# Kernel optimization log

Hardware: AMD Instinct MI355X
Metric: run time of the kernel (lower is better)

## Reference

```python
import jax, jax.numpy as jnp
import numpy as np

ALPHA = 0.1
DEPTH = 10
N_NODES = 100000
N_EDGES = 1600000
FEATS = 512
HIDDEN = 64
CLASSES = 64


def setup_inputs() -> dict:
    key = jax.random.key(0)
    k1, k2, k3, k4 = jax.random.split(key, 4)
    x = jax.random.normal(k1, (N_NODES, FEATS), dtype=jnp.float32)
    edges = jax.random.randint(k2, (2, N_EDGES), 0, N_NODES, dtype=jnp.int64)
    W1 = jax.random.normal(k3, (FEATS, HIDDEN), dtype=jnp.float32) * (1.0 / np.sqrt(FEATS))
    b1 = jnp.zeros((HIDDEN,), dtype=jnp.float32)
    W2 = jax.random.normal(k4, (HIDDEN, CLASSES), dtype=jnp.float32) * (1.0 / np.sqrt(HIDDEN))
    b2 = jnp.zeros((CLASSES,), dtype=jnp.float32)
    return {"x": x, "edges": edges, "W1": W1, "b1": b1, "W2": W2, "b2": b2}


def reference(x, edges, W1, b1, W2, b2):
    src, dst = edges[0], edges[1]
    # symmetric GCN normalization from edge list (in-degree over dst)
    deg = jax.ops.segment_sum(jnp.ones((N_EDGES,), jnp.float32), dst,
                              num_segments=N_NODES)
    deg = jnp.maximum(deg, 1.0)
    inv_sqrt_deg = jax.lax.rsqrt(deg)
    norm = inv_sqrt_deg[src] * inv_sqrt_deg[dst]  # [E]

    # MLP: feats -> hidden -> classes (dropout = identity in eval mode)
    h = jax.nn.relu(x @ W1 + b1)
    h = h @ W2 + b2
    h0 = h

    for _ in range(DEPTH):
        msgs = h[src] * norm[:, None]                     # [E, C] gather
        agg = jax.ops.segment_sum(msgs, dst, num_segments=N_NODES)  # scatter-add
        h = agg * (1.0 - ALPHA) + ALPHA * h0
    return h
```

## Files before the change

kernel.cpp:

```cpp
#include <hip/hip_runtime.h>
#include <hip/hip_fp16.h>

#define FEATS 512
#define HIDDEN 64
#define CLASSES 64
#define DEPTH 10
#define ALPHA 0.1f

#define BUCKET_BITS 8
#define BUCKET 256
#define NB_C 391
#define K3_CHUNK 8192
#define K3_THREADS 512

typedef __attribute__((ext_vector_type(8))) short short8;
typedef __attribute__((ext_vector_type(4))) float f32x4;

__device__ __forceinline__ unsigned short bf16_hi(float f) {
    unsigned u = __float_as_uint(f);
    unsigned r = u + 0x7FFF + ((u >> 16) & 1);
    return (unsigned short)(r >> 16);
}
__device__ __forceinline__ float bf16_tof(unsigned short h) {
    return __uint_as_float(((unsigned)h) << 16);
}

__global__ __launch_bounds__(256) void bucket_hist_kernel(const int* __restrict__ dst,
                                                          int* __restrict__ bcnt,
                                                          int NB, int E) {
    __shared__ int h[NB_C];
    for (int j = threadIdx.x; j < NB; j += 256) h[j] = 0;
    __syncthreads();
    int i = blockIdx.x * 256 + threadIdx.x;
    int stride = gridDim.x * 256;
    for (; i < E; i += stride) atomicAdd(&h[dst[i] >> BUCKET_BITS], 1);
    __syncthreads();
    for (int j = threadIdx.x; j < NB; j += 256) {
        int v = h[j];
        if (v) atomicAdd(&bcnt[j], v);
    }
}

__global__ __launch_bounds__(1024) void bucket_scan_kernel(const int* __restrict__ bcnt,
                                                           int* __restrict__ bptr,
                                                           int* __restrict__ gcur,
                                                           int* __restrict__ rowptr,
                                                           int NB, int N, int E) {
    __shared__ int sd[1024];
    int t = threadIdx.x;
    int i0 = 2 * t, i1 = 2 * t + 1;
    int a = (i0 < NB) ? bcnt[i0] : 0;
    int b = (i1 < NB) ? bcnt[i1] : 0;
    int s = a + b;
    sd[t] = s;
    __syncthreads();
    for (int off = 1; off < 1024; off <<= 1) {
        int v = (t >= off) ? sd[t - off] : 0;
        __syncthreads();
        sd[t] += v;
        __syncthreads();
    }
    int excl = sd[t] - s;
    if (i0 < NB) { bptr[i0] = excl;     gcur[i0] = excl; }
    if (i1 < NB) { bptr[i1] = excl + a; gcur[i1] = excl + a; }
    if (t == 0) { bptr[NB] = E; rowptr[N] = E; }
}

__global__ __launch_bounds__(K3_THREADS) void bucket_scatter_kernel(const int* __restrict__ src,
                                                                    const int* __restrict__ dst,
                                                                    int* __restrict__ gcur,
                                                                    int* __restrict__ part,
                                                                    int NB, int E) {
    __shared__ int hist[NB_C];
    __shared__ int base[NB_C];
    int cbase = blockIdx.x * K3_CHUNK;
    for (int j = threadIdx.x; j < NB; j += K3_THREADS) hist[j] = 0;
    __syncthreads();
    for (int k = 0; k < K3_CHUNK; k += K3_THREADS) {
        int i = cbase + k + threadIdx.x;
        if (i < E) atomicAdd(&hist[dst[i] >> BUCKET_BITS], 1);
    }
    __syncthreads();
    for (int j = threadIdx.x; j < NB; j += K3_THREADS) {
        int h = hist[j];
        base[j] = (h > 0) ? atomicAdd(&gcur[j], h) : 0;
        hist[j] = 0;
    }
    __syncthreads();
    for (int k = 0; k < K3_CHUNK; k += K3_THREADS) {
        int i = cbase + k + threadIdx.x;
        if (i < E) {
            int d = dst[i];
            int j = d >> BUCKET_BITS;
            int off = atomicAdd(&hist[j], 1);
            part[(size_t)(base[j] + off)] = (src[i] << BUCKET_BITS) | (d & (BUCKET - 1));
        }
    }
}

__global__ __launch_bounds__(256) void part_to_csr_kernel(const int* __restrict__ bptr,
                                                          const int* __restrict__ part,
                                                          int* __restrict__ rowptr,
                                                          float* __restrict__ inv_sqrt,
                                                          int* __restrict__ csr_src,
                                                          int N) {
    __shared__ int cnt[BUCKET];
    __shared__ int cur[BUCKET];
    __shared__ int wsum[4];
    int b = blockIdx.x;
    int lo = b << BUCKET_BITS;
    int tid = threadIdx.x;
    int p0 = bptr[b], p1 = bptr[b + 1];
    cnt[tid] = 0;
    __syncthreads();
    for (int i = p0 + tid; i < p1; i += 256) {
        atomicAdd(&cnt[part[i] & (BUCKET - 1)], 1);
    }
    __syncthreads();
    {
        int wv = tid >> 6, ln = tid & 63;
        int v = cnt[tid];
        int incl = v;
#pragma unroll
        for (int off = 1; off < 64; off <<= 1) {
            int t = __shfl_up(incl, off);
            if (ln >= off) incl += t;
        }
        if (ln == 63) wsum[wv] = incl;
        __syncthreads();
        int woff = 0;
#pragma unroll
        for (int w = 0; w < 4; ++w)
            if (w < wv) woff += wsum[w];
        int excl = woff + incl - v;
        if (lo + tid < N) {
            rowptr[lo + tid] = p0 + excl;
            inv_sqrt[lo + tid] = rsqrtf((float)(v < 1 ? 1 : v));
        }
        cur[tid] = excl;
    }
    __syncthreads();
    for (int i = p0 + tid; i < p1; i += 256) {
        int pe = part[i];
        int off = atomicAdd(&cur[pe & (BUCKET - 1)], 1);
        csr_src[p0 + off] = ((unsigned)pe) >> BUCKET_BITS;
    }
}

__global__ __launch_bounds__(256) void pack_w_kernel(const float* __restrict__ W1,
                                                     const float* __restrict__ W2,
                                                     unsigned short* __restrict__ w1h,
                                                     unsigned short* __restrict__ w1l,
                                                     unsigned short* __restrict__ w2h,
                                                     unsigned short* __restrict__ w2l) {
    int id = blockIdx.x * blockDim.x + threadIdx.x;
    if (id < 4096) {
        int lane = id & 63, f = (id >> 6) & 3, ks = id >> 8;
        int col = f * 16 + (lane & 15);
        int k0 = ks * 32 + (lane >> 4) * 8;
#pragma unroll
        for (int i = 0; i < 8; ++i) {
            float v = W1[(k0 + i) * HIDDEN + col];
            unsigned short h = bf16_hi(v);
            w1h[id * 8 + i] = h;
            w1l[id * 8 + i] = bf16_hi(v - bf16_tof(h));
        }
    } else if (id < 4096 + 512) {
        int p = id - 4096;
        int lane = p & 63, f = (p >> 6) & 3, ks = p >> 8;
        int col = f * 16 + (lane & 15);
        int k0 = ks * 32 + (lane >> 4) * 8;
#pragma unroll
        for (int i = 0; i < 8; ++i) {
            float v = W2[(k0 + i) * CLASSES + col];
            unsigned short h = bf16_hi(v);
            w2h[p * 8 + i] = h;
            w2l[p * 8 + i] = bf16_hi(v - bf16_tof(h));
        }
    }
}

__global__ __launch_bounds__(256) void mlp_mfma_kernel(const float* __restrict__ x,
                                                       const unsigned short* __restrict__ w1h,
                                                       const unsigned short* __restrict__ w1l,
                                                       const float* __restrict__ b1,
                                                       const unsigned short* __restrict__ w2h,
                                                       const unsigned short* __restrict__ w2l,
                                                       const float* __restrict__ b2,
                                                       const float* __restrict__ is,
                                                       __half* __restrict__ h0h,
                                                       __half* __restrict__ u0,
                                                       int N) {
    __shared__ float hs[4][16][68];
    int wave = threadIdx.x >> 6;
    int lane = threadIdx.x & 63;
    int tile = blockIdx.x * 4 + wave;
    if (tile * 16 >= N) return;

    int row = lane & 15;
    int koff = (lane >> 4) * 8;
    const short8* w1hv = (const short8*)w1h;
    const short8* w1lv = (const short8*)w1l;
    const short8* w2hv = (const short8*)w2h;
    const short8* w2lv = (const short8*)w2l;

    f32x4 c[4] = {};
    const float* xrow = x + (size_t)(tile * 16 + row) * FEATS + koff;
#pragma unroll 4
    for (int ks = 0; ks < 16; ++ks) {
        float4 a0 = *(const float4*)(xrow + ks * 32);
        float4 a1 = *(const float4*)(xrow + ks * 32 + 4);
        float av[8] = {a0.x, a0.y, a0.z, a0.w, a1.x, a1.y, a1.z, a1.w};
        short8 ah, al;
#pragma unroll
        for (int j = 0; j < 8; ++j) {
            unsigned short h = bf16_hi(av[j]);
            ah[j] = (short)h;
            al[j] = (short)bf16_hi(av[j] - bf16_tof(h));
        }
#pragma unroll
        for (int f = 0; f < 4; ++f) {
            short8 bh = w1hv[(ks * 4 + f) * 64 + lane];
            short8 bl = w1lv[(ks * 4 + f) * 64 + lane];
            c[f] = __builtin_amdgcn_mfma_f32_16x16x32_bf16(ah, bh, c[f], 0, 0, 0);
            c[f] = __builtin_amdgcn_mfma_f32_16x16x32_bf16(ah, bl, c[f], 0, 0, 0);
            c[f] = __builtin_amdgcn_mfma_f32_16x16x32_bf16(al, bh, c[f], 0, 0, 0);
        }
    }
#pragma unroll
    for (int f = 0; f < 4; ++f) {
        float bias = b1[f * 16 + (lane & 15)];
#pragma unroll
        for (int r = 0; r < 4; ++r) {
            hs[wave][(lane >> 4) * 4 + r][f * 16 + (lane & 15)] = fmaxf(c[f][r] + bias, 0.0f);
        }
    }

    f32x4 c2[4] = {};
#pragma unroll
    for (int ks = 0; ks < 2; ++ks) {
        float4 a0 = *(const float4*)&hs[wave][row][ks * 32 + koff];
        float4 a1 = *(const float4*)&hs[wave][row][ks * 32 + koff + 4];
        float av[8] = {a0.x, a0.y, a0.z, a0.w, a1.x, a1.y, a1.z, a1.w};
        short8 ah, al;
#pragma unroll
        for (int j = 0; j < 8; ++j) {
            unsigned short h = bf16_hi(av[j]);
            ah[j] = (short)h;
            al[j] = (short)bf16_hi(av[j] - bf16_tof(h));
        }
#pragma unroll
        for (int f = 0; f < 4; ++f) {
            short8 bh = w2hv[(ks * 4 + f) * 64 + lane];
            short8 bl = w2lv[(ks * 4 + f) * 64 + lane];
            c2[f] = __builtin_amdgcn_mfma_f32_16x16x32_bf16(ah, bh, c2[f], 0, 0, 0);
            c2[f] = __builtin_amdgcn_mfma_f32_16x16x32_bf16(ah, bl, c2[f], 0, 0, 0);
            c2[f] = __builtin_amdgcn_mfma_f32_16x16x32_bf16(al, bh, c2[f], 0, 0, 0);
        }
    }
    float isv[4];
#pragma unroll
    for (int r = 0; r < 4; ++r) {
        int n = tile * 16 + (lane >> 4) * 4 + r;
        isv[r] = is[n];
    }
#pragma unroll
    for (int f = 0; f < 4; ++f) {
        float bias = b2[f * 16 + (lane & 15)];
#pragma unroll
        for (int r = 0; r < 4; ++r) {
            int n = tile * 16 + (lane >> 4) * 4 + r;
            float v = c2[f][r] + bias;
            h0h[(size_t)n * CLASSES + f * 16 + (lane & 15)] = __float2half(v);
            u0[(size_t)n * CLASSES + f * 16 + (lane & 15)] = __float2half(v * isv[r]);
        }
    }
}

__global__ __launch_bounds__(256) void prop_kernel(const int* __restrict__ rowptr,
                                                   const int* __restrict__ csr_src,
                                                   const float* __restrict__ is,
                                                   const __half* __restrict__ u_in,
                                                   const __half* __restrict__ h0h,
                                                   __half* __restrict__ u_out,
                                                   float* __restrict__ out_f32,
                                                   int N, int last) {
    int wid = (blockIdx.x * blockDim.x + threadIdx.x) >> 6;
    int lane = threadIdx.x & 63;
    if (wid >= N) return;
    int base = rowptr[wid];
    int end = rowptr[wid + 1];
    int grp = lane >> 3, sub = lane & 7;

    float isd = is[wid];
    size_t rowo = ((size_t)wid << 6) + (sub << 3);
    uint4 hq = make_uint4(0, 0, 0, 0);
    if (grp == 0) hq = *(const uint4*)(h0h + rowo);

    float acc[8] = {0.f, 0.f, 0.f, 0.f, 0.f, 0.f, 0.f, 0.f};
    for (int b = base; b < end; b += 16) {
        int e0 = b + grp;
        int e1 = e0 + 8;
        bool v0 = e0 < end;
        bool v1 = e1 < end;
        uint4 q0, q1;
        int s0, s1;
        if (v0) s0 = csr_src[e0];
        if (v1) s1 = csr_src[e1];
        if (v0) q0 = *(const uint4*)(u_in + ((size_t)s0 << 6) + (sub << 3));
        if (v1) q1 = *(const uint4*)(u_in + ((size_t)s1 << 6) + (sub << 3));
        if (v0) {
            const __half2* hp = (const __half2*)&q0;
#pragma unroll
            for (int k = 0; k < 4; ++k) {
                float2 f2 = __half22float2(hp[k]);
                acc[2 * k] += f2.x;
                acc[2 * k + 1] += f2.y;
            }
        }
        if (v1) {
            const __half2* hp = (const __half2*)&q1;
#pragma unroll
            for (int k = 0; k < 4; ++k) {
                float2 f2 = __half22float2(hp[k]);
                acc[2 * k] += f2.x;
                acc[2 * k + 1] += f2.y;
            }
        }
    }
#pragma unroll
    for (int j = 0; j < 8; ++j) {
        acc[j] += __shfl_xor(acc[j], 8);
        acc[j] += __shfl_xor(acc[j], 16);
        acc[j] += __shfl_xor(acc[j], 32);
    }
    if (grp == 0) {
        const __half2* hp = (const __half2*)&hq;
        float h[8];
#pragma unroll
        for (int k = 0; k < 4; ++k) {
            float2 f2 = __half22float2(hp[k]);
            h[2 * k] = f2.x;
            h[2 * k + 1] = f2.y;
        }
        if (last) {
            float r[8];
#pragma unroll
            for (int j = 0; j < 8; ++j) r[j] = (1.0f - ALPHA) * isd * acc[j] + ALPHA * h[j];
            *(float4*)(out_f32 + rowo) = make_float4(r[0], r[1], r[2], r[3]);
            *(float4*)(out_f32 + rowo + 4) = make_float4(r[4], r[5], r[6], r[7]);
        } else {
            __half2 w[4];
#pragma unroll
            for (int k = 0; k < 4; ++k) {
                float a = ((1.0f - ALPHA) * isd * acc[2 * k] + ALPHA * h[2 * k]) * isd;
                float b = ((1.0f - ALPHA) * isd * acc[2 * k + 1] + ALPHA * h[2 * k + 1]) * isd;
                w[k] = __floats2half2_rn(a, b);
            }
            *(uint4*)(u_out + rowo) = *(uint4*)w;
        }
    }
}

extern "C" void kernel_launch(void* const* d_in, const int* in_sizes, int n_in,
                              void* d_out, int out_size, void* d_ws, size_t ws_size,
                              hipStream_t stream) {
    const float* x = (const float*)d_in[0];
    const int* edges = (const int*)d_in[1];
    const float* W1 = (const float*)d_in[2];
    const float* b1 = (const float*)d_in[3];
    const float* W2 = (const float*)d_in[4];
    const float* b2 = (const float*)d_in[5];
    float* out = (float*)d_out;

    const int N = in_sizes[0] / FEATS;
    const int E = in_sizes[1] / 2;
    const int NB = (N + BUCKET - 1) >> BUCKET_BITS;
    const int* src = edges;
    const int* dst = edges + E;

    char* ws = (char*)d_ws;
    size_t off = 0;
    auto alloc = [&](size_t bytes) {
        char* p = ws + off;
        off = (off + bytes + 255) & ~(size_t)255;
        return p;
    };
    int* part = (int*)alloc((size_t)E * 4);
    int* csr_src = (int*)alloc((size_t)E * 4);
    int* bcnt = (int*)alloc((size_t)NB * 4);
    int* bptr = (int*)alloc((size_t)(NB + 1) * 4);
    int* gcur = (int*)alloc((size_t)NB * 4);
    int* rowptr = (int*)alloc((size_t)(N + 1) * 4);
    float* inv_sqrt = (float*)alloc((size_t)N * 4);
    __half* h0h = (__half*)alloc((size_t)N * CLASSES * 2);
    __half* uA = (__half*)alloc((size_t)N * CLASSES * 2);
    __half* uB = (__half*)alloc((size_t)N * CLASSES * 2);
    unsigned short* w1h = (unsigned short*)alloc(4096 * 8 * 2);
    unsigned short* w1l = (unsigned short*)alloc(4096 * 8 * 2);
    unsigned short* w2h = (unsigned short*)alloc(512 * 8 * 2);
    unsigned short* w2l = (unsigned short*)alloc(512 * 8 * 2);
    (void)ws_size;

    hipMemsetAsync(bcnt, 0, (size_t)NB * 4, stream);
    bucket_hist_kernel<<<128, 256, 0, stream>>>(dst, bcnt, NB, E);
    bucket_scan_kernel<<<1, 1024, 0, stream>>>(bcnt, bptr, gcur, rowptr, NB, N, E);
    int k3_blocks = (E + K3_CHUNK - 1) / K3_CHUNK;
    bucket_scatter_kernel<<<k3_blocks, K3_THREADS, 0, stream>>>(src, dst, gcur, part, NB, E);
    part_to_csr_kernel<<<NB, 256, 0, stream>>>(bptr, part, rowptr, inv_sqrt, csr_src, N);

    pack_w_kernel<<<18, 256, 0, stream>>>(W1, W2, w1h, w1l, w2h, w2l);
    int tiles = (N + 15) / 16;
    mlp_mfma_kernel<<<(tiles + 3) / 4, 256, 0, stream>>>(x, w1h, w1l, b1, w2h, w2l, b2,
                                                         inv_sqrt, h0h, uA, N);

    int blocks = (N * 64 + 255) / 256;
    for (int d = 0; d < DEPTH; ++d) {
        const __half* uin = (d & 1) ? uB : uA;
        __half* uout = (d & 1) ? uA : uB;
        int last = (d == DEPTH - 1);
        prop_kernel<<<blocks, 256, 0, stream>>>(rowptr, csr_src, inv_sqrt, uin, h0h,
                                                uout, out, N, last);
    }
}
```

Baseline: 549.6 us.

## Partition CSR edges into source-range quarters for gather locality

Builds the CSR with an extra partition on source-node range (4 quarters of 32768 nodes), so edges are grouped by src quarter first and then by dst bucket. Each prop kernel wave walks four per-quarter row segments in turn, which is meant to keep the gathered u_in rows for a phase inside a smaller working set that fits better in L2/MALL cache. In exchange it adds a separate norm kernel, four times as many bucket counters and part_to_csr blocks, and more loop overhead and short segments per node in prop.

Result: slower. 790.0 us (+43.7%).

```diff
diff --git a/kernel.cpp b/kernel.cpp
--- a/kernel.cpp
+++ b/kernel.cpp
@@ -10,6 +10,9 @@
 #define BUCKET_BITS 8
 #define BUCKET 256
 #define NB_C 391
+#define NQT 4
+#define QT_SHIFT 15
+#define NK_C (NQT * NB_C)
 #define K3_CHUNK 8192
 #define K3_THREADS 512
 
@@ -25,17 +28,21 @@
     return __uint_as_float(((unsigned)h) << 16);
 }
 
-__global__ __launch_bounds__(256) void bucket_hist_kernel(const int* __restrict__ dst,
+__global__ __launch_bounds__(256) void bucket_hist_kernel(const int* __restrict__ src,
+                                                          const int* __restrict__ dst,
                                                           int* __restrict__ bcnt,
-                                                          int NB, int E) {
-    __shared__ int h[NB_C];
-    for (int j = threadIdx.x; j < NB; j += 256) h[j] = 0;
+                                                          int NB, int NK, int E) {
+    __shared__ int h[NK_C];
+    for (int j = threadIdx.x; j < NK; j += 256) h[j] = 0;
     __syncthreads();
     int i = blockIdx.x * 256 + threadIdx.x;
     int stride = gridDim.x * 256;
-    for (; i < E; i += stride) atomicAdd(&h[dst[i] >> BUCKET_BITS], 1);
-    __syncthreads();
-    for (int j = threadIdx.x; j < NB; j += 256) {
+    for (; i < E; i += stride) {
+        int kq = (src[i] >> QT_SHIFT) * NB + (dst[i] >> BUCKET_BITS);
+        atomicAdd(&h[kq], 1);
+    }
+    __syncthreads();
+    for (int j = threadIdx.x; j < NK; j += 256) {
         int v = h[j];
         if (v) atomicAdd(&bcnt[j], v);
     }
@@ -44,13 +51,13 @@
 __global__ __launch_bounds__(1024) void bucket_scan_kernel(const int* __restrict__ bcnt,
                                                            int* __restrict__ bptr,
                                                            int* __restrict__ gcur,
-                                                           int* __restrict__ rowptr,
-                                                           int NB, int N, int E) {
+                                                           int* __restrict__ rowq,
+                                                           int NB, int NK, int N, int E) {
     __shared__ int sd[1024];
     int t = threadIdx.x;
     int i0 = 2 * t, i1 = 2 * t + 1;
-    int a = (i0 < NB) ? bcnt[i0] : 0;
-    int b = (i1 < NB) ? bcnt[i1] : 0;
+    int a = (i0 < NK) ? bcnt[i0] : 0;
+    int b = (i1 < NK) ? bcnt[i1] : 0;
     int s = a + b;
     sd[t] = s;
     __syncthreads();
@@ -61,27 +68,32 @@
         __syncthreads();
     }
     int excl = sd[t] - s;
-    if (i0 < NB) { bptr[i0] = excl;     gcur[i0] = excl; }
-    if (i1 < NB) { bptr[i1] = excl + a; gcur[i1] = excl + a; }
-    if (t == 0) { bptr[NB] = E; rowptr[N] = E; }
+    if (i0 < NK) { bptr[i0] = excl;     gcur[i0] = excl; }
+    if (i1 < NK) { bptr[i1] = excl + a; gcur[i1] = excl + a; }
+    if (t == 0) bptr[NK] = E;
+    __syncthreads();
+    if (t < NQT) rowq[t * (N + 1) + N] = bptr[(t + 1) * NB];
 }
 
 __global__ __launch_bounds__(K3_THREADS) void bucket_scatter_kernel(const int* __restrict__ src,
                                                                     const int* __restrict__ dst,
                                                                     int* __restrict__ gcur,
                                                                     int* __restrict__ part,
-                                                                    int NB, int E) {
-    __shared__ int hist[NB_C];
-    __shared__ int base[NB_C];
+                                                                    int NB, int NK, int E) {
+    __shared__ int hist[NK_C];
+    __shared__ int base[NK_C];
     int cbase = blockIdx.x * K3_CHUNK;
-    for (int j = threadIdx.x; j < NB; j += K3_THREADS) hist[j] = 0;
+    for (int j = threadIdx.x; j < NK; j += K3_THREADS) hist[j] = 0;
     __syncthreads();
     for (int k = 0; k < K3_CHUNK; k += K3_THREADS) {
         int i = cbase + k + threadIdx.x;
-        if (i < E) atomicAdd(&hist[dst[i] >> BUCKET_BITS], 1);
-    }
-    __syncthreads();
-    for (int j = threadIdx.x; j < NB; j += K3_THREADS) {
+        if (i < E) {
+            int kq = (src[i] >> QT_SHIFT) * NB + (dst[i] >> BUCKET_BITS);
+            atomicAdd(&hist[kq], 1);
+        }
+    }
+    __syncthreads();
+    for (int j = threadIdx.x; j < NK; j += K3_THREADS) {
         int h = hist[j];
         base[j] = (h > 0) ? atomicAdd(&gcur[j], h) : 0;
         hist[j] = 0;
@@ -90,27 +102,28 @@
     for (int k = 0; k < K3_CHUNK; k += K3_THREADS) {
         int i = cbase + k + threadIdx.x;
         if (i < E) {
-            int d = dst[i];
-            int j = d >> BUCKET_BITS;
-            int off = atomicAdd(&hist[j], 1);
-            part[(size_t)(base[j] + off)] = (src[i] << BUCKET_BITS) | (d & (BUCKET - 1));
+            int sv = src[i], d = dst[i];
+            int kq = (sv >> QT_SHIFT) * NB + (d >> BUCKET_BITS);
+            int off = atomicAdd(&hist[kq], 1);
+            part[(size_t)(base[kq] + off)] = (sv << BUCKET_BITS) | (d & (BUCKET - 1));
         }
     }
 }
 
 __global__ __launch_bounds__(256) void part_to_csr_kernel(const int* __restrict__ bptr,
                                                           const int* __restrict__ part,
-                                                          int* __restrict__ rowptr,
-                                                          float* __restrict__ inv_sqrt,
+                                                          int* __restrict__ rowq,
                                                           int* __restrict__ csr_src,
-                                                          int N) {
+                                                          int NB, int N) {
     __shared__ int cnt[BUCKET];
     __shared__ int cur[BUCKET];
     __shared__ int wsum[4];
-    int b = blockIdx.x;
-    int lo = b << BUCKET_BITS;
+    int kb = blockIdx.x;
+    int qt = kb / NB;
+    int bb = kb - qt * NB;
+    int lo = bb << BUCKET_BITS;
     int tid = threadIdx.x;
-    int p0 = bptr[b], p1 = bptr[b + 1];
+    int p0 = bptr[kb], p1 = bptr[kb + 1];
     cnt[tid] = 0;
     __syncthreads();
     for (int i = p0 + tid; i < p1; i += 256) {
@@ -133,10 +146,7 @@
         for (int w = 0; w < 4; ++w)
             if (w < wv) woff += wsum[w];
         int excl = woff + incl - v;
-        if (lo + tid < N) {
-            rowptr[lo + tid] = p0 + excl;
-            inv_sqrt[lo + tid] = rsqrtf((float)(v < 1 ? 1 : v));
-        }
+        if (lo + tid < N) rowq[qt * (N + 1) + lo + tid] = p0 + excl;
         cur[tid] = excl;
     }
     __syncthreads();
@@ -145,6 +155,18 @@
         int off = atomicAdd(&cur[pe & (BUCKET - 1)], 1);
         csr_src[p0 + off] = ((unsigned)pe) >> BUCKET_BITS;
     }
+}
+
+__global__ __launch_bounds__(256) void norm_kernel(const int* __restrict__ rowq,
+                                                   float* __restrict__ inv_sqrt, int N) {
+    int i = blockIdx.x * 256 + threadIdx.x;
+    if (i >= N) return;
+    int deg = 0;
+#pragma unroll
+    for (int q = 0; q < NQT; ++q) {
+        deg += rowq[q * (N + 1) + i + 1] - rowq[q * (N + 1) + i];
+    }
+    inv_sqrt[i] = rsqrtf((float)(deg < 1 ? 1 : deg));
 }
 
 __global__ __launch_bounds__(256) void pack_w_kernel(const float* __restrict__ W1,
@@ -277,7 +299,7 @@
     }
 }
 
-__global__ __launch_bounds__(256) void prop_kernel(const int* __restrict__ rowptr,
+__global__ __launch_bounds__(256) void prop_kernel(const int* __restrict__ rowq,
                                                    const int* __restrict__ csr_src,
                                                    const float* __restrict__ is,
                                                    const __half* __restrict__ u_in,
@@ -288,8 +310,6 @@
     int wid = (blockIdx.x * blockDim.x + threadIdx.x) >> 6;
     int lane = threadIdx.x & 63;
     if (wid >= N) return;
-    int base = rowptr[wid];
-    int end = rowptr[wid + 1];
     int grp = lane >> 3, sub = lane & 7;
 
     float isd = is[wid];
@@ -298,33 +318,37 @@
     if (grp == 0) hq = *(const uint4*)(h0h + rowo);
 
     float acc[8] = {0.f, 0.f, 0.f, 0.f, 0.f, 0.f, 0.f, 0.f};
-    for (int b = base; b < end; b += 16) {
-        int e0 = b + grp;
-        int e1 = e0 + 8;
-        bool v0 = e0 < end;
-        bool v1 = e1 < end;
-        uint4 q0, q1;
-        int s0, s1;
-        if (v0) s0 = csr_src[e0];
-        if (v1) s1 = csr_src[e1];
-        if (v0) q0 = *(const uint4*)(u_in + ((size_t)s0 << 6) + (sub << 3));
-        if (v1) q1 = *(const uint4*)(u_in + ((size_t)s1 << 6) + (sub << 3));
-        if (v0) {
-            const __half2* hp = (const __half2*)&q0;
-#pragma unroll
-            for (int k = 0; k < 4; ++k) {
-                float2 f2 = __half22float2(hp[k]);
-                acc[2 * k] += f2.x;
-                acc[2 * k + 1] += f2.y;
+    for (int qt = 0; qt < NQT; ++qt) {
+        int base = rowq[qt * (N + 1) + wid];
+        int end = rowq[qt * (N + 1) + wid + 1];
+        for (int b = base; b < end; b += 16) {
+            int e0 = b + grp;
+            int e1 = e0 + 8;
+            bool v0 = e0 < end;
+            bool v1 = e1 < end;
+            uint4 q0, q1;
+            int s0, s1;
+            if (v0) s0 = csr_src[e0];
+            if (v1) s1 = csr_src[e1];
+            if (v0) q0 = *(const uint4*)(u_in + ((size_t)s0 << 6) + (sub << 3));
+            if (v1) q1 = *(const uint4*)(u_in + ((size_t)s1 << 6) + (sub << 3));
+            if (v0) {
+                const __half2* hp = (const __half2*)&q0;
+#pragma unroll
+                for (int k = 0; k < 4; ++k) {
+                    float2 f2 = __half22float2(hp[k]);
+                    acc[2 * k] += f2.x;
+                    acc[2 * k + 1] += f2.y;
+                }
             }
-        }
-        if (v1) {
-            const __half2* hp = (const __half2*)&q1;
-#pragma unroll
-            for (int k = 0; k < 4; ++k) {
-                float2 f2 = __half22float2(hp[k]);
-                acc[2 * k] += f2.x;
-                acc[2 * k + 1] += f2.y;
+            if (v1) {
+                const __half2* hp = (const __half2*)&q1;
+#pragma unroll
+                for (int k = 0; k < 4; ++k) {
+                    float2 f2 = __half22float2(hp[k]);
+                    acc[2 * k] += f2.x;
+                    acc[2 * k + 1] += f2.y;
+                }
             }
         }
     }
@@ -376,6 +400,7 @@
     const int N = in_sizes[0] / FEATS;
     const int E = in_sizes[1] / 2;
     const int NB = (N + BUCKET - 1) >> BUCKET_BITS;
+    const int NK = NQT * NB;
     const int* src = edges;
     const int* dst = edges + E;
 
@@ -388,10 +413,10 @@
     };
     int* part = (int*)alloc((size_t)E * 4);
     int* csr_src = (int*)alloc((size_t)E * 4);
-    int* bcnt = (int*)alloc((size_t)NB * 4);
-    int* bptr = (int*)alloc((size_t)(NB + 1) * 4);
-    int* gcur = (int*)alloc((size_t)NB * 4);
-    int* rowptr = (int*)alloc((size_t)(N + 1) * 4);
+    int* bcnt = (int*)alloc((size_t)NK * 4);
+    int* bptr = (int*)alloc((size_t)(NK + 1) * 4);
+    int* gcur = (int*)alloc((size_t)NK * 4);
+    int* rowq = (int*)alloc((size_t)NQT * (N + 1) * 4);
     float* inv_sqrt = (float*)alloc((size_t)N * 4);
     __half* h0h = (__half*)alloc((size_t)N * CLASSES * 2);
     __half* uA = (__half*)alloc((size_t)N * CLASSES * 2);
@@ -402,12 +427,13 @@
     unsigned short* w2l = (unsigned short*)alloc(512 * 8 * 2);
     (void)ws_size;
 
-    hipMemsetAsync(bcnt, 0, (size_t)NB * 4, stream);
-    bucket_hist_kernel<<<128, 256, 0, stream>>>(dst, bcnt, NB, E);
-    bucket_scan_kernel<<<1, 1024, 0, stream>>>(bcnt, bptr, gcur, rowptr, NB, N, E);
+    hipMemsetAsync(bcnt, 0, (size_t)NK * 4, stream);
+    bucket_hist_kernel<<<128, 256, 0, stream>>>(src, dst, bcnt, NB, NK, E);
+    bucket_scan_kernel<<<1, 1024, 0, stream>>>(bcnt, bptr, gcur, rowq, NB, NK, N, E);
     int k3_blocks = (E + K3_CHUNK - 1) / K3_CHUNK;
-    bucket_scatter_kernel<<<k3_blocks, K3_THREADS, 0, stream>>>(src, dst, gcur, part, NB, E);
-    part_to_csr_kernel<<<NB, 256, 0, stream>>>(bptr, part, rowptr, inv_sqrt, csr_src, N);
+    bucket_scatter_kernel<<<k3_blocks, K3_THREADS, 0, stream>>>(src, dst, gcur, part, NB, NK, E);
+    part_to_csr_kernel<<<NK, 256, 0, stream>>>(bptr, part, rowq, csr_src, NB, N);
+    norm_kernel<<<(N + 255) / 256, 256, 0, stream>>>(rowq, inv_sqrt, N);
 
     pack_w_kernel<<<18, 256, 0, stream>>>(W1, W2, w1h, w1l, w2h, w2l);
     int tiles = (N + 15) / 16;
@@ -419,7 +445,7 @@
         const __half* uin = (d & 1) ? uB : uA;
         __half* uout = (d & 1) ? uA : uB;
         int last = (d == DEPTH - 1);
-        prop_kernel<<<blocks, 256, 0, stream>>>(rowptr, csr_src, inv_sqrt, uin, h0h,
+        prop_kernel<<<blocks, 256, 0, stream>>>(rowq, csr_src, inv_sqrt, uin, h0h,
                                                 uout, out, N, last);
     }
 }
```
